# Performance work log

Hardware: AMD Instinct MI355X
Metric: run time of the kernel (lower is better)

The kernel has to match this reference:

```python
import jax, jax.numpy as jnp
import numpy as np

HEADS = 8
IH, IW = 32, 32
C_IN, C_OUT = 512, 512


def setup_inputs() -> dict:
    key = jax.random.key(0)
    k1, k2, k3, k4, k5 = jax.random.split(key, 5)
    B = 32
    n = IH + IW + (IH // 2) * (IW // 2)  # pooled kv length = 320
    x = jax.random.normal(k1, (B, C_IN, IH, IW), dtype=jnp.float32)
    # 1x1 conv weights stored as [out, in] (bias-free qkv, biased output proj)
    Wqkv = jax.random.normal(k2, (3 * C_IN, C_IN), dtype=jnp.float32) * 0.02
    Wout = jax.random.normal(k3, (C_OUT, C_IN), dtype=jnp.float32) * 0.02
    bout = jnp.zeros((C_OUT,), dtype=jnp.float32)
    pos_embed = jax.random.normal(k4, (1, IH * IW, n), dtype=jnp.float32) * 0.2
    return {"x": x, "Wqkv": Wqkv, "Wout": Wout, "bout": bout, "pos_embed": pos_embed}


def _pool_gate(t, B, C, H, W):
    # adaptive_avg_pool2d(.,(None,1)) == mean over width -> [B,C,H]
    th = t.mean(axis=3)
    # adaptive_avg_pool2d(.,(1,None)) (+permute) == mean over height -> [B,C,W]
    tw = t.mean(axis=2)
    # adaptive_avg_pool2d to (H//2, W//2) with even dims == 2x2 average pooling
    tp = t.reshape(B, C, H // 2, 2, W // 2, 2).mean(axis=(3, 5)).reshape(B, C, -1)
    s = jax.nn.sigmoid(jnp.concatenate([th, tw, tp], axis=2))  # [B,C,n]
    d = C // HEADS
    # 'b (h d) n -> b h n d'
    return s.reshape(B, HEADS, d, -1).transpose(0, 1, 3, 2)


def reference(x, Wqkv, Wout, bout, pos_embed):
    B, C, H, W = x.shape
    d = C // HEADS
    scale = d ** (-0.5)
    qkv = jnp.einsum('bchw,oc->bohw', x, Wqkv)  # 1x1 conv, no bias
    q, k, v = jnp.split(qkv, 3, axis=1)
    # 'b (h d) ih iw -> b h (ih iw) d'
    q = q.reshape(B, HEADS, d, H * W).transpose(0, 1, 3, 2)
    k = _pool_gate(k, B, C, H, W)  # [B,h,n,d]
    v = _pool_gate(v, B, C, H, W)  # [B,h,n,d]
    dots = jnp.einsum('bhsd,bhnd->bhsn', q, k) * scale + pos_embed  # pos_embed [1,s,n] broadcasts
    attn = jax.nn.softmax(dots, axis=-1)
    out = jnp.einsum('bhsn,bhnd->bhsd', attn, v)
    # 'b h (ih iw) d -> b (h d) ih iw'
    out = out.transpose(0, 1, 3, 2).reshape(B, HEADS * d, H, W)
    out = jnp.einsum('bchw,oc->bohw', out, Wout) + bout[None, :, None, None]
    return out
```

## Files before the change

### kernel.cpp

```cpp
#include <hip/hip_runtime.h>
#include <hip/hip_bf16.h>
#include <math.h>

#define HEADS 8
#define CH    512
#define S     1024
#define NKV   320
#define DH    64
#define BATCH 32

typedef __attribute__((ext_vector_type(8))) short short8;
typedef __attribute__((ext_vector_type(4))) short short4v;
typedef __attribute__((ext_vector_type(4))) float float4v;

__device__ __forceinline__ short f2bf(float f) {
    __hip_bfloat16 h = __float2bfloat16(f);
    return *reinterpret_cast<short*>(&h);
}

#define GLOAD_LDS16(gp, lp) __builtin_amdgcn_global_load_lds( \
    (const __attribute__((address_space(1))) void*)(gp),      \
    (__attribute__((address_space(3))) void*)(lp), 16, 0, 0)

__global__ __launch_bounds__(256) void pool_kernel(const float* __restrict__ x,
                                                   float* __restrict__ xp) {
    __shared__ float sm[4][1024];
    const int w = threadIdx.x >> 6;
    const int l = threadIdx.x & 63;
    const int p = blockIdx.x * 4 + w;
    const float* src = x + (size_t)p * 1024;
    #pragma unroll
    for (int j = 0; j < 16; ++j) sm[w][j * 64 + l] = src[j * 64 + l];
    __syncthreads();
    float* dst = xp + (size_t)p * NKV;
    const float* pl = sm[w];
    #pragma unroll
    for (int g = 0; g < 5; ++g) {
        const int nn = g * 64 + l;
        float r;
        if (nn < 32) {
            const int h = nn; float s = 0.f;
            #pragma unroll
            for (int ww = 0; ww < 32; ++ww) s += pl[h * 32 + ww];
            r = s * (1.0f / 32.0f);
        } else if (nn < 64) {
            const int ww = nn - 32; float s = 0.f;
            #pragma unroll
            for (int h = 0; h < 32; ++h) s += pl[h * 32 + ww];
            r = s * (1.0f / 32.0f);
        } else {
            const int i = nn - 64;
            const int ph = i >> 4, pw = i & 15;
            r = 0.25f * (pl[(2 * ph) * 32 + 2 * pw]     + pl[(2 * ph) * 32 + 2 * pw + 1] +
                         pl[(2 * ph + 1) * 32 + 2 * pw] + pl[(2 * ph + 1) * 32 + 2 * pw + 1]);
        }
        dst[nn] = r;
    }
}

__global__ __launch_bounds__(256) void tcast(const float* __restrict__ in,
                                             short* __restrict__ out, int R, int C) {
    __shared__ float sm[64][65];
    const int t = threadIdx.x;
    const int c0 = blockIdx.x * 64, r0 = blockIdx.y * 64;
    const float* ib = in + ((size_t)blockIdx.z * R + r0) * C + c0;
    #pragma unroll
    for (int rep = 0; rep < 4; ++rep) {
        const int r = rep * 16 + (t >> 4), c = (t & 15) * 4;
        const float4 v = *(const float4*)&ib[(size_t)r * C + c];
        sm[r][c] = v.x; sm[r][c + 1] = v.y; sm[r][c + 2] = v.z; sm[r][c + 3] = v.w;
    }
    __syncthreads();
    short* ob = out + ((size_t)blockIdx.z * C + c0) * R + r0;
    #pragma unroll
    for (int rep = 0; rep < 4; ++rep) {
        const int cr = rep * 16 + (t >> 4), rc = (t & 15) * 4;
        short4v p;
        #pragma unroll
        for (int e = 0; e < 4; ++e) p[e] = f2bf(sm[rc + e][cr]);
        *(short4v*)&ob[(size_t)cr * R + rc] = p;
    }
}

__global__ __launch_bounds__(256) void castw(const float* __restrict__ in,
                                             short* __restrict__ out, int n) {
    const int i = (blockIdx.x * 256 + threadIdx.x) * 4;
    if (i < n) {
        const float4 v = *(const float4*)&in[i];
        short4v p = {f2bf(v.x), f2bf(v.y), f2bf(v.z), f2bf(v.w)};
        *(short4v*)&out[i] = p;
    }
}

template <int MT, int NT, int ACT, typename OT>
__global__ __launch_bounds__(256) void gemm_bf16(const short* __restrict__ A, long sAb,
                                                 const short* __restrict__ B, long sBb,
                                                 const float* __restrict__ bias,
                                                 OT* __restrict__ C, int M, int N) {
    constexpr int K  = 512;
    constexpr int BM = 32 * MT, BN = 32 * NT;
    __shared__ short As[BM * 64];
    __shared__ short Bs[BN * 64];
    const int t = threadIdx.x, w = t >> 6, l = t & 63;
    const int wm = w >> 1, wn = w & 1, quad = l >> 4, m15 = l & 15;
    const int bz = blockIdx.z;
    const int n0 = blockIdx.x * BN, m0 = blockIdx.y * BM;
    const short* gA = A + (size_t)sAb * bz + (size_t)m0 * K;
    const short* gB = B + (size_t)sBb * bz + (size_t)n0 * K;
    const int lrow = l >> 3;
    const int pc   = l & 7;

    const float4v zf = {0.f, 0.f, 0.f, 0.f};
    float4v acc[MT][NT];
    #pragma unroll
    for (int i = 0; i < MT; ++i)
        #pragma unroll
        for (int j = 0; j < NT; ++j) acc[i][j] = zf;

    for (int k0 = 0; k0 < K; k0 += 64) {
        #pragma unroll
        for (int ii = w; ii < BM / 8; ii += 4) {
            const int row = ii * 8 + lrow;
            const int x = pc ^ (row & 7);
            GLOAD_LDS16(gA + (size_t)row * K + k0 + x * 8, &As[ii * 512]);
        }
        #pragma unroll
        for (int ii = w; ii < BN / 8; ii += 4) {
            const int row = ii * 8 + lrow;
            const int x = pc ^ (row & 7);
            GLOAD_LDS16(gB + (size_t)row * K + k0 + x * 8, &Bs[ii * 512]);
        }
        __syncthreads();
        #pragma unroll
        for (int ks = 0; ks < 2; ++ks) {
            const int xa = (((ks * 4 + quad) ^ (m15 & 7))) * 8;
            short8 aF[MT], bF[NT];
            #pragma unroll
            for (int i = 0; i < MT; ++i)
                aF[i] = *(const short8*)&As[((wm * MT + i) * 16 + m15) * 64 + xa];
            #pragma unroll
            for (int j = 0; j < NT; ++j)
                bF[j] = *(const short8*)&Bs[((wn * NT + j) * 16 + m15) * 64 + xa];
            #pragma unroll
            for (int i = 0; i < MT; ++i)
                #pragma unroll
                for (int j = 0; j < NT; ++j)
                    acc[i][j] = __builtin_amdgcn_mfma_f32_16x16x32_bf16(aF[i], bF[j], acc[i][j], 0, 0, 0);
        }
        __syncthreads();
    }

    OT* gC = C + (size_t)bz * M * N;
    #pragma unroll
    for (int i = 0; i < MT; ++i) {
        #pragma unroll
        for (int r = 0; r < 4; ++r) {
            const int row = m0 + (wm * MT + i) * 16 + quad * 4 + r;
            float bv = 0.f;
            if (ACT == 2) bv = bias[row];
            #pragma unroll
            for (int j = 0; j < NT; ++j) {
                const int col = n0 + (wn * NT + j) * 16 + m15;
                float v = acc[i][j][r];
                if (ACT == 1) { v = 1.0f / (1.0f + __expf(-v)); if (col < 512) v *= 0.125f; }
                if (ACT == 2) v += bv;
                if constexpr (sizeof(OT) == 2)
                    ((short*)gC)[(size_t)row * N + col] = f2bf(v);
                else
                    ((float*)gC)[(size_t)row * N + col] = v;
            }
        }
    }
}

__global__ __launch_bounds__(512) void attn_mfma(const short* __restrict__ qT,
                                                 const short* __restrict__ kvT,
                                                 const float* __restrict__ pos,
                                                 short* __restrict__ aoT) {
    __shared__ short smP[8 * 16 * 72];
    __shared__ short smB[64 * 344];
    const int tid = threadIdx.x, w = tid >> 6, l = tid & 63;
    const int quad = l >> 4, m15 = l & 15;
    const int b = blockIdx.z, h = blockIdx.y, s0 = blockIdx.x * 128;
    const short* kvb = kvT + (size_t)b * NKV * 1024;

    for (int i2 = w; i2 < 40; i2 += 8) {
        const int nb = i2 % 5, dg = i2 / 5;
        GLOAD_LDS16(kvb + (size_t)(nb * 64 + l) * 1024 + h * 64 + dg * 8,
                    &smB[(dg * 320 + nb * 64) * 8]);
    }
    const short* qb = qT + (size_t)(b * S + s0 + w * 16 + m15) * 512 + h * 64;
    const short8 aQ0 = *(const short8*)&qb[quad * 8];
    const short8 aQ1 = *(const short8*)&qb[32 + quad * 8];
    __syncthreads();

    const float4v zf = {0.f, 0.f, 0.f, 0.f};
    float4v acc[20];
    #pragma unroll
    for (int tt = 0; tt < 20; ++tt) acc[tt] = zf;

    #pragma unroll
    for (int tt = 0; tt < 20; ++tt) {
        const short8 b0 = *(const short8*)&smB[(quad * 320 + tt * 16 + m15) * 8];
        const short8 b1 = *(const short8*)&smB[((4 + quad) * 320 + tt * 16 + m15) * 8];
        acc[tt] = __builtin_amdgcn_mfma_f32_16x16x32_bf16(aQ0, b0, acc[tt], 0, 0, 0);
        acc[tt] = __builtin_amdgcn_mfma_f32_16x16x32_bf16(aQ1, b1, acc[tt], 0, 0, 0);
    }

    const int srow = s0 + w * 16 + quad * 4;
    float mrow[4] = {-1e30f, -1e30f, -1e30f, -1e30f};
    #pragma unroll
    for (int tt = 0; tt < 20; ++tt) {
        #pragma unroll
        for (int r = 0; r < 4; ++r) {
            const float sc = acc[tt][r] + pos[(size_t)(srow + r) * NKV + tt * 16 + m15];
            acc[tt][r] = sc;
            mrow[r] = fmaxf(mrow[r], sc);
        }
    }
    #pragma unroll
    for (int r = 0; r < 4; ++r) {
        #pragma unroll
        for (int off = 1; off < 16; off <<= 1)
            mrow[r] = fmaxf(mrow[r], __shfl_xor(mrow[r], off, 16));
    }
    float lrow[4] = {0.f, 0.f, 0.f, 0.f};
    #pragma unroll
    for (int tt = 0; tt < 20; ++tt) {
        #pragma unroll
        for (int r = 0; r < 4; ++r) {
            const float p = __expf(acc[tt][r] - mrow[r]);
            acc[tt][r] = p;
            lrow[r] += p;
        }
    }
    #pragma unroll
    for (int r = 0; r < 4; ++r) {
        #pragma unroll
        for (int off = 1; off < 16; off <<= 1)
            lrow[r] += __shfl_xor(lrow[r], off, 16);
    }

    __syncthreads();

    for (int it = 0; it < 5; ++it) {
        const int i2 = it * 512 + tid;
        const int n5 = i2 & 31, d8 = (i2 >> 5) & 7, nb = i2 >> 8;
        const int n = nb * 32 + n5;
        const short8 v = *(const short8*)&kvb[(size_t)n * 1024 + 512 + h * 64 + d8 * 8];
        #pragma unroll
        for (int e = 0; e < 8; ++e) smB[(d8 * 8 + e) * 344 + n] = v[e];
    }
    __syncthreads();

    short* Pw = &smP[w * 16 * 72];
    float4v O[4];
    #pragma unroll
    for (int dt = 0; dt < 4; ++dt) O[dt] = zf;
    #pragma unroll
    for (int c = 0; c < 5; ++c) {
        #pragma unroll
        for (int tt = 0; tt < 4; ++tt) {
            #pragma unroll
            for (int r = 0; r < 4; ++r)
                Pw[(quad * 4 + r) * 72 + tt * 16 + m15] = f2bf(acc[4 * c + tt][r]);
        }
        #pragma unroll
        for (int ks = 0; ks < 2; ++ks) {
            const short8 aP = *(const short8*)&Pw[m15 * 72 + ks * 32 + quad * 8];
            #pragma unroll
            for (int dt = 0; dt < 4; ++dt) {
                const short8 bV = *(const short8*)&smB[(dt * 16 + m15) * 344 + c * 64 + ks * 32 + quad * 8];
                O[dt] = __builtin_amdgcn_mfma_f32_16x16x32_bf16(aP, bV, O[dt], 0, 0, 0);
            }
        }
    }

    float inv[4];
    #pragma unroll
    for (int r = 0; r < 4; ++r) inv[r] = 1.0f / lrow[r];
    #pragma unroll
    for (int dt = 0; dt < 4; ++dt) {
        #pragma unroll
        for (int r = 0; r < 4; ++r) {
            const int s = s0 + w * 16 + quad * 4 + r;
            aoT[(size_t)(b * S + s) * 512 + h * 64 + dt * 16 + m15] = f2bf(O[dt][r] * inv[r]);
        }
    }
}

extern "C" void kernel_launch(void* const* d_in, const int* in_sizes, int n_in,
                              void* d_out, int out_size, void* d_ws, size_t ws_size,
                              hipStream_t stream) {
    const float* x    = (const float*)d_in[0];
    const float* Wqkv = (const float*)d_in[1];
    const float* Wout = (const float*)d_in[2];
    const float* bout = (const float*)d_in[3];
    const float* pos  = (const float*)d_in[4];
    char* ws = (char*)d_ws;
    float* xp   = (float*)(ws + 0);
    short* xT   = (short*)(ws + 20971520);
    short* xpT  = (short*)(ws + 54525952);
    short* qT   = (short*)(ws + 65011712);
    short* kvT  = (short*)(ws + 98566144);
    short* aoT  = (short*)(ws + 119537664);
    short* Wbf  = (short*)(ws + 153092096);
    short* Wobf = (short*)(ws + 154664960);
    float* out  = (float*)d_out;

    castw<<<dim3(768), 256, 0, stream>>>(Wqkv, Wbf, 1536 * 512);
    castw<<<dim3(256), 256, 0, stream>>>(Wout, Wobf, 512 * 512);
    pool_kernel<<<dim3(BATCH * CH / 4), 256, 0, stream>>>(x, xp);
    tcast<<<dim3(16, 8, BATCH), 256, 0, stream>>>(x, xT, CH, S);
    tcast<<<dim3(5, 8, BATCH), 256, 0, stream>>>(xp, xpT, CH, NKV);
    gemm_bf16<4, 4, 0, short><<<dim3(4, 8, BATCH), 256, 0, stream>>>(
        xT, (long)S * CH, Wbf, 0, nullptr, qT, S, CH);
    gemm_bf16<2, 8, 1, short><<<dim3(4, 5, BATCH), 256, 0, stream>>>(
        xpT, (long)NKV * CH, Wbf + CH * CH, 0, nullptr, kvT, NKV, 2 * CH);
    attn_mfma<<<dim3(8, HEADS, BATCH), 512, 0, stream>>>(qT, kvT, pos, aoT);
    gemm_bf16<4, 4, 2, float><<<dim3(8, 4, BATCH), 256, 0, stream>>>(
        Wobf, 0, aoT, (long)S * CH, bout, out, CH, S);
}
```

Baseline: 309.6 us.

## Fuse pooling and transpose-cast into one prep kernel; bf16 pos; prefetch V

Replaces the separate pool, fp32 intermediate and two transpose-cast kernels with a single prep kernel. It reads x once, writes the bf16 transpose and computes the pooled features from the bf16 tile in shared memory. The positional embedding is cast to bf16 once per call so attention reads half the bytes. Attention now prefetches V into registers before the QK/softmax phase, and its launch bounds are raised. Pooling from bf16-rounded values and bf16 pos reduce accuracy slightly, and the prep grid has only 256 blocks, which may underuse the GPU.

```diff
diff --git a/kernel.cpp b/kernel.cpp
--- a/kernel.cpp
+++ b/kernel.cpp
@@ -17,70 +17,15 @@
     __hip_bfloat16 h = __float2bfloat16(f);
     return *reinterpret_cast<short*>(&h);
 }
+__device__ __forceinline__ float bf2f(short s) {
+    union { int i; float f; } u;
+    u.i = ((int)(unsigned short)s) << 16;
+    return u.f;
+}
 
 #define GLOAD_LDS16(gp, lp) __builtin_amdgcn_global_load_lds( \
     (const __attribute__((address_space(1))) void*)(gp),      \
     (__attribute__((address_space(3))) void*)(lp), 16, 0, 0)
-
-__global__ __launch_bounds__(256) void pool_kernel(const float* __restrict__ x,
-                                                   float* __restrict__ xp) {
-    __shared__ float sm[4][1024];
-    const int w = threadIdx.x >> 6;
-    const int l = threadIdx.x & 63;
-    const int p = blockIdx.x * 4 + w;
-    const float* src = x + (size_t)p * 1024;
-    #pragma unroll
-    for (int j = 0; j < 16; ++j) sm[w][j * 64 + l] = src[j * 64 + l];
-    __syncthreads();
-    float* dst = xp + (size_t)p * NKV;
-    const float* pl = sm[w];
-    #pragma unroll
-    for (int g = 0; g < 5; ++g) {
-        const int nn = g * 64 + l;
-        float r;
-        if (nn < 32) {
-            const int h = nn; float s = 0.f;
-            #pragma unroll
-            for (int ww = 0; ww < 32; ++ww) s += pl[h * 32 + ww];
-            r = s * (1.0f / 32.0f);
-        } else if (nn < 64) {
-            const int ww = nn - 32; float s = 0.f;
-            #pragma unroll
-            for (int h = 0; h < 32; ++h) s += pl[h * 32 + ww];
-            r = s * (1.0f / 32.0f);
-        } else {
-            const int i = nn - 64;
-            const int ph = i >> 4, pw = i & 15;
-            r = 0.25f * (pl[(2 * ph) * 32 + 2 * pw]     + pl[(2 * ph) * 32 + 2 * pw + 1] +
-                         pl[(2 * ph + 1) * 32 + 2 * pw] + pl[(2 * ph + 1) * 32 + 2 * pw + 1]);
-        }
-        dst[nn] = r;
-    }
-}
-
-__global__ __launch_bounds__(256) void tcast(const float* __restrict__ in,
-                                             short* __restrict__ out, int R, int C) {
-    __shared__ float sm[64][65];
-    const int t = threadIdx.x;
-    const int c0 = blockIdx.x * 64, r0 = blockIdx.y * 64;
-    const float* ib = in + ((size_t)blockIdx.z * R + r0) * C + c0;
-    #pragma unroll
-    for (int rep = 0; rep < 4; ++rep) {
-        const int r = rep * 16 + (t >> 4), c = (t & 15) * 4;
-        const float4 v = *(const float4*)&ib[(size_t)r * C + c];
-        sm[r][c] = v.x; sm[r][c + 1] = v.y; sm[r][c + 2] = v.z; sm[r][c + 3] = v.w;
-    }
-    __syncthreads();
-    short* ob = out + ((size_t)blockIdx.z * C + c0) * R + r0;
-    #pragma unroll
-    for (int rep = 0; rep < 4; ++rep) {
-        const int cr = rep * 16 + (t >> 4), rc = (t & 15) * 4;
-        short4v p;
-        #pragma unroll
-        for (int e = 0; e < 4; ++e) p[e] = f2bf(sm[rc + e][cr]);
-        *(short4v*)&ob[(size_t)cr * R + rc] = p;
-    }
-}
 
 __global__ __launch_bounds__(256) void castw(const float* __restrict__ in,
                                              short* __restrict__ out, int n) {
@@ -89,6 +34,70 @@
         const float4 v = *(const float4*)&in[i];
         short4v p = {f2bf(v.x), f2bf(v.y), f2bf(v.z), f2bf(v.w)};
         *(short4v*)&out[i] = p;
+    }
+}
+
+__global__ __launch_bounds__(256) void prep(const float* __restrict__ x,
+                                            short* __restrict__ xT,
+                                            short* __restrict__ xpT) {
+    __shared__ short sm[64 * 260];
+    const int t = threadIdx.x, lane = t & 63, w = t >> 6;
+    const int b = blockIdx.y, cg = blockIdx.x;
+    const float* xb = x + ((size_t)(b * 512 + cg * 64)) * 1024;
+    short* xTb = xT + ((size_t)b * 1024) * 512 + cg * 64;
+    short* xpb = xpT + ((size_t)b * 320) * 512 + cg * 64;
+    float twacc[8];
+    #pragma unroll
+    for (int j = 0; j < 8; ++j) twacc[j] = 0.f;
+
+    for (int ci = 0; ci < 4; ++ci) {
+        const int hw0 = ci * 256;
+        #pragma unroll
+        for (int i = 0; i < 16; ++i) {
+            const int c = i * 4 + w;
+            const float4 v = *(const float4*)&xb[(size_t)c * 1024 + hw0 + lane * 4];
+            short4v p = {f2bf(v.x), f2bf(v.y), f2bf(v.z), f2bf(v.w)};
+            *(short4v*)&sm[c * 260 + lane * 4] = p;
+        }
+        __syncthreads();
+        {
+            short rowv[64];
+            #pragma unroll
+            for (int c = 0; c < 64; ++c) rowv[c] = sm[c * 260 + t];
+            short* dst = &xTb[(size_t)(hw0 + t) * 512];
+            #pragma unroll
+            for (int v8 = 0; v8 < 8; ++v8)
+                *(short8*)&dst[v8 * 8] = *(short8*)&rowv[v8 * 8];
+        }
+        #pragma unroll
+        for (int hh = 0; hh < 2; ++hh) {
+            const int h = w * 2 + hh;
+            float s = 0.f;
+            #pragma unroll
+            for (int ww = 0; ww < 32; ++ww) s += bf2f(sm[lane * 260 + h * 32 + ww]);
+            xpb[(size_t)(ci * 8 + h) * 512 + lane] = f2bf(s * (1.0f / 32.0f));
+        }
+        #pragma unroll
+        for (int j = 0; j < 8; ++j) {
+            const int ww = w * 8 + j;
+            float s = 0.f;
+            #pragma unroll
+            for (int h = 0; h < 8; ++h) s += bf2f(sm[lane * 260 + h * 32 + ww]);
+            twacc[j] += s;
+        }
+        #pragma unroll
+        for (int pw = 0; pw < 16; ++pw) {
+            const int base = lane * 260 + (w * 2) * 32 + pw * 2;
+            const float s = bf2f(sm[base]) + bf2f(sm[base + 1]) +
+                            bf2f(sm[base + 32]) + bf2f(sm[base + 33]);
+            xpb[(size_t)(64 + (ci * 4 + w) * 16 + pw) * 512 + lane] = f2bf(s * 0.25f);
+        }
+        __syncthreads();
+    }
+    #pragma unroll
+    for (int j = 0; j < 8; ++j) {
+        const int ww = w * 8 + j;
+        xpb[(size_t)(32 + ww) * 512 + lane] = f2bf(twacc[j] * (1.0f / 32.0f));
     }
 }
 
@@ -121,14 +130,14 @@
         #pragma unroll
         for (int ii = w; ii < BM / 8; ii += 4) {
             const int row = ii * 8 + lrow;
-            const int x = pc ^ (row & 7);
-            GLOAD_LDS16(gA + (size_t)row * K + k0 + x * 8, &As[ii * 512]);
+            const int xx = pc ^ (row & 7);
+            GLOAD_LDS16(gA + (size_t)row * K + k0 + xx * 8, &As[ii * 512]);
         }
         #pragma unroll
         for (int ii = w; ii < BN / 8; ii += 4) {
             const int row = ii * 8 + lrow;
-            const int x = pc ^ (row & 7);
-            GLOAD_LDS16(gB + (size_t)row * K + k0 + x * 8, &Bs[ii * 512]);
+            const int xx = pc ^ (row & 7);
+            GLOAD_LDS16(gB + (size_t)row * K + k0 + xx * 8, &Bs[ii * 512]);
         }
         __syncthreads();
         #pragma unroll
@@ -173,10 +182,10 @@
     }
 }
 
-__global__ __launch_bounds__(512) void attn_mfma(const short* __restrict__ qT,
-                                                 const short* __restrict__ kvT,
-                                                 const float* __restrict__ pos,
-                                                 short* __restrict__ aoT) {
+__global__ __launch_bounds__(512, 4) void attn_mfma(const short* __restrict__ qT,
+                                                    const short* __restrict__ kvT,
+                                                    const short* __restrict__ posb,
+                                                    short* __restrict__ aoT) {
     __shared__ short smP[8 * 16 * 72];
     __shared__ short smB[64 * 344];
     const int tid = threadIdx.x, w = tid >> 6, l = tid & 63;
@@ -189,6 +198,16 @@
         GLOAD_LDS16(kvb + (size_t)(nb * 64 + l) * 1024 + h * 64 + dg * 8,
                     &smB[(dg * 320 + nb * 64) * 8]);
     }
+    short8 vpf[5];
+    int vn[5], vd8[5];
+    #pragma unroll
+    for (int it = 0; it < 5; ++it) {
+        const int i2 = it * 512 + tid;
+        const int n5 = i2 & 31, d8 = (i2 >> 5) & 7, nb = i2 >> 8;
+        const int n = nb * 32 + n5;
+        vn[it] = n; vd8[it] = d8;
+        vpf[it] = *(const short8*)&kvb[(size_t)n * 1024 + 512 + h * 64 + d8 * 8];
+    }
     const short* qb = qT + (size_t)(b * S + s0 + w * 16 + m15) * 512 + h * 64;
     const short8 aQ0 = *(const short8*)&qb[quad * 8];
     const short8 aQ1 = *(const short8*)&qb[32 + quad * 8];
@@ -213,7 +232,7 @@
     for (int tt = 0; tt < 20; ++tt) {
         #pragma unroll
         for (int r = 0; r < 4; ++r) {
-            const float sc = acc[tt][r] + pos[(size_t)(srow + r) * NKV + tt * 16 + m15];
+            const float sc = acc[tt][r] + bf2f(posb[(size_t)(srow + r) * NKV + tt * 16 + m15]);
             acc[tt][r] = sc;
             mrow[r] = fmaxf(mrow[r], sc);
         }
@@ -243,13 +262,11 @@
 
     __syncthreads();
 
+    #pragma unroll
     for (int it = 0; it < 5; ++it) {
-        const int i2 = it * 512 + tid;
-        const int n5 = i2 & 31, d8 = (i2 >> 5) & 7, nb = i2 >> 8;
-        const int n = nb * 32 + n5;
-        const short8 v = *(const short8*)&kvb[(size_t)n * 1024 + 512 + h * 64 + d8 * 8];
-        #pragma unroll
-        for (int e = 0; e < 8; ++e) smB[(d8 * 8 + e) * 344 + n] = v[e];
+        #pragma unroll
+        for (int e = 0; e < 8; ++e)
+            smB[(vd8[it] * 8 + e) * 344 + vn[it]] = vpf[it][e];
     }
     __syncthreads();
 
@@ -298,26 +315,25 @@
     const float* bout = (const float*)d_in[3];
     const float* pos  = (const float*)d_in[4];
     char* ws = (char*)d_ws;
-    float* xp   = (float*)(ws + 0);
-    short* xT   = (short*)(ws + 20971520);
-    short* xpT  = (short*)(ws + 54525952);
-    short* qT   = (short*)(ws + 65011712);
-    short* kvT  = (short*)(ws + 98566144);
-    short* aoT  = (short*)(ws + 119537664);
-    short* Wbf  = (short*)(ws + 153092096);
-    short* Wobf = (short*)(ws + 154664960);
+    short* xT   = (short*)(ws + 0);
+    short* xpT  = (short*)(ws + 33554432);
+    short* qT   = (short*)(ws + 44040192);
+    short* kvT  = (short*)(ws + 77594624);
+    short* aoT  = (short*)(ws + 98566144);
+    short* Wbf  = (short*)(ws + 132120576);
+    short* Wobf = (short*)(ws + 133693440);
+    short* posb = (short*)(ws + 134217728);
     float* out  = (float*)d_out;
 
     castw<<<dim3(768), 256, 0, stream>>>(Wqkv, Wbf, 1536 * 512);
     castw<<<dim3(256), 256, 0, stream>>>(Wout, Wobf, 512 * 512);
-    pool_kernel<<<dim3(BATCH * CH / 4), 256, 0, stream>>>(x, xp);
-    tcast<<<dim3(16, 8, BATCH), 256, 0, stream>>>(x, xT, CH, S);
-    tcast<<<dim3(5, 8, BATCH), 256, 0, stream>>>(xp, xpT, CH, NKV);
+    castw<<<dim3(320), 256, 0, stream>>>(pos, posb, S * NKV);
+    prep<<<dim3(8, BATCH), 256, 0, stream>>>(x, xT, xpT);
     gemm_bf16<4, 4, 0, short><<<dim3(4, 8, BATCH), 256, 0, stream>>>(
         xT, (long)S * CH, Wbf, 0, nullptr, qT, S, CH);
     gemm_bf16<2, 8, 1, short><<<dim3(4, 5, BATCH), 256, 0, stream>>>(
         xpT, (long)NKV * CH, Wbf + CH * CH, 0, nullptr, kvT, NKV, 2 * CH);
-    attn_mfma<<<dim3(8, HEADS, BATCH), 512, 0, stream>>>(qT, kvT, pos, aoT);
+    attn_mfma<<<dim3(8, HEADS, BATCH), 512, 0, stream>>>(qT, kvT, posb, aoT);
     gemm_bf16<4, 4, 2, float><<<dim3(8, 4, BATCH), 256, 0, stream>>>(
         Wobf, 0, aoT, (long)S * CH, bout, out, CH, S);
 }
```

After: 345.6 us. +11.6%, slower.
